# Kernel optimization log

Hardware: AMD Instinct MI355X
Metric: run time of the kernel (lower is better)

The kernel has to match this reference:

```python
import jax, jax.numpy as jnp
import numpy as np

MIN_CONTEXT_SIZE = 64
FUTURE_STEPS = 12


def setup_inputs() -> dict:
    key = jax.random.key(0)
    k1, k2, k3 = jax.random.split(key, 3)
    B, T, E, C = 32, 256, 256, 256
    embeddings = jax.random.normal(k1, (B, T, E), dtype=jnp.float32)
    contexts = jax.random.normal(k2, (B, T, C), dtype=jnp.float32)
    # Bilinear comparator weight, scaled like a typical linear init
    W = jax.random.normal(k3, (E, C), dtype=jnp.float32) * (1.0 / np.sqrt(E).astype(np.float32))
    return {"embeddings": embeddings, "contexts": contexts, "W": W}


def reference(embeddings, contexts, W):
    B, T, E = embeddings.shape
    log_probs = []
    for step in range(FUTURE_STEPS):
        emb = embeddings[:, MIN_CONTEXT_SIZE + step:T]          # (B, S, E)
        ctx = contexts[:, MIN_CONTEXT_SIZE - 1:T - step - 1]    # (B, S, C)
        S = T - step - MIN_CONTEXT_SIZE
        # all-pairs bilinear scores: score[b,s,j,t] = emb[b,s] @ W @ ctx[j,t]
        proj = jnp.einsum('bse,ec->bsc', emb, W)                # (B, S, C)
        scores = jnp.einsum('bsc,jtc->bsjt', proj, ctx)         # (B, S, B, S)
        flat = scores.reshape(B * S, B * S)
        positives = jnp.diagonal(flat).reshape(B, S)            # matched (b,s) pairs
        lse = jax.nn.logsumexp(scores.reshape(B, S, B * S), axis=-1)
        lse = lse - jnp.log(jnp.asarray(B * S, dtype=scores.dtype))
        log_probs.append((positives - lse).reshape(-1))
    flat_log_probs = jnp.concatenate(log_probs, axis=0)
    return -flat_log_probs.mean()
```

## Files before the change

kernel.cpp:

```cpp
#include <hip/hip_runtime.h>
#include <hip/hip_bf16.h>


#define NROW 6144
#define TAIL0 181
#define NTERMS 71616.0f

typedef __attribute__((ext_vector_type(8))) short short8;
typedef __attribute__((ext_vector_type(4))) float f32x4;

__device__ __forceinline__ ushort f2bf(float f) {
  union { float f; uint32_t u; } v; v.f = f;
  uint32_t u = v.u;
  return (ushort)((u + 0x7FFFu + ((u >> 16) & 1u)) >> 16);
}
__device__ __forceinline__ float b2f(ushort h) {
  union { uint32_t u; float f; } v; v.u = ((uint32_t)h) << 16; return v.f;
}

__device__ __forceinline__ void gload16(const ushort* g, ushort* l) {
  __builtin_amdgcn_global_load_lds((const __attribute__((address_space(1))) void*)g,
                                   (__attribute__((address_space(3))) void*)l, 16, 0, 0);
}

__global__ void k_castW(const float* __restrict__ W, ushort* __restrict__ Wt) {
  int c = blockIdx.x, e = threadIdx.x;
  Wt[c * 256 + e] = f2bf(W[e * 256 + c]);
}

__global__ void k_castX(const float* __restrict__ ctx, ushort* __restrict__ X) {
  int c = blockIdx.x;
  int j = c & 31, t = c >> 5;
  const float4* src = (const float4*)(ctx + ((size_t)(j * 256 + 63 + t)) * 256);
  float4 f = src[threadIdx.x];
  ushort4 o;
  o.x = f2bf(f.x); o.y = f2bf(f.y); o.z = f2bf(f.z); o.w = f2bf(f.w);
  ((ushort4*)(X + (size_t)c * 256))[threadIdx.x] = o;
}

__global__ __launch_bounds__(256) void k_proj(const float* __restrict__ emb,
                                              const ushort* __restrict__ Wt,
                                              ushort* __restrict__ P) {
  __shared__ ushort Al[16 * 256];
  int tid = threadIdx.x;
  int rt = blockIdx.x;
#pragma unroll
  for (int q = 0; q < 4; ++q) {
    int cc = tid + q * 256;
    int rw = cc >> 6, f4 = cc & 63;
    int u = rt * 16 + rw, b = u / 192, urow = u - b * 192;
    float4 f = *(const float4*)(emb + ((size_t)(b * 256 + 64 + urow)) * 256 + f4 * 4);
    ushort4 o;
    o.x = f2bf(f.x); o.y = f2bf(f.y); o.z = f2bf(f.z); o.w = f2bf(f.w);
    int c8 = f4 >> 1;
    *(ushort4*)&Al[rw * 256 + ((c8 ^ (rw & 7)) * 8) + (f4 & 1) * 4] = o;
  }
  __syncthreads();

  int w = tid >> 6, l = tid & 63;
  int fr = l & 15, kb = l >> 4;
  short8 af[8];
#pragma unroll
  for (int kk = 0; kk < 8; ++kk) {
    int c8 = kk * 4 + kb;
    af[kk] = *(const short8*)&Al[fr * 256 + (c8 ^ (fr & 7)) * 8];
  }
#pragma unroll
  for (int i = 0; i < 4; ++i) {
    int ct = w * 4 + i;
    const short8* bp = (const short8*)(Wt + (size_t)(ct * 16 + fr) * 256);
    f32x4 acc = {0.f, 0.f, 0.f, 0.f};
#pragma unroll
    for (int kk = 0; kk < 8; ++kk)
      acc = __builtin_amdgcn_mfma_f32_16x16x32_bf16(af[kk], bp[kk * 4 + kb], acc, 0, 0, 0);
#pragma unroll
    for (int r = 0; r < 4; ++r)
      P[(size_t)(rt * 16 + kb * 4 + r) * 256 + ct * 16 + fr] = f2bf(acc[r]);
  }
}

__global__ __launch_bounds__(256) void k_scores(const ushort* __restrict__ P,
                                                const ushort* __restrict__ X,
                                                float* __restrict__ sum0,
                                                float* __restrict__ tail,
                                                float* __restrict__ pos) {
  __shared__ ushort Al[128 * 32];
  __shared__ ushort Bl[128 * 32];
  int tid = threadIdx.x;
  int w = tid >> 6, l = tid & 63;
  int wr = w >> 1, wc = w & 1;
  int rowbase = blockIdx.x * 128;
  int colbase = blockIdx.y * 128;

  int c0 = w * 128 + l;
  int r0 = c0 >> 2, s0 = (c0 & 3) ^ ((c0 >> 3) & 3);
  int c1 = c0 + 64;
  int r1 = c1 >> 2, s1 = (c1 & 3) ^ ((c1 >> 3) & 3);
  const ushort* gA0 = P + (size_t)(rowbase + r0) * 256 + s0 * 8;
  const ushort* gA1 = P + (size_t)(rowbase + r1) * 256 + s1 * 8;
  const ushort* gB0 = X + (size_t)(colbase + r0) * 256 + s0 * 8;
  const ushort* gB1 = X + (size_t)(colbase + r1) * 256 + s1 * 8;
  ushort* lA0 = Al + (size_t)(w * 128) * 8;
  ushort* lA1 = Al + (size_t)(w * 128 + 64) * 8;
  ushort* lB0 = Bl + (size_t)(w * 128) * 8;
  ushort* lB1 = Bl + (size_t)(w * 128 + 64) * 8;

  int fr = l & 15, kb = l >> 4;
  int kbs = kb ^ ((fr >> 1) & 3);

  f32x4 acc[4][4];
#pragma unroll
  for (int m = 0; m < 4; ++m)
#pragma unroll
    for (int n = 0; n < 4; ++n) acc[m][n] = {0.f, 0.f, 0.f, 0.f};

  for (int kk = 0; kk < 8; ++kk) {
    gload16(gA0 + kk * 32, lA0);
    gload16(gA1 + kk * 32, lA1);
    gload16(gB0 + kk * 32, lB0);
    gload16(gB1 + kk * 32, lB1);
    __syncthreads();

    short8 af[4], bf[4];
#pragma unroll
    for (int m = 0; m < 4; ++m)
      af[m] = *(const short8*)&Al[(wr * 64 + m * 16 + fr) * 32 + kbs * 8];
#pragma unroll
    for (int n = 0; n < 4; ++n)
      bf[n] = *(const short8*)&Bl[(wc * 64 + n * 16 + fr) * 32 + kbs * 8];
#pragma unroll
    for (int m = 0; m < 4; ++m)
#pragma unroll
      for (int n = 0; n < 4; ++n)
        acc[m][n] = __builtin_amdgcn_mfma_f32_16x16x32_bf16(af[m], bf[n], acc[m][n], 0, 0, 0);
    if (kk < 7) __syncthreads();
  }

  int t0g = blockIdx.y * 4 + wc * 2;
#pragma unroll
  for (int m = 0; m < 4; ++m) {
    int rowg = rowbase + wr * 64 + m * 16 + kb * 4;
#pragma unroll
    for (int r = 0; r < 4; ++r) {
      int u = rowg + r;
      int b = u / 192;
      int urow = u - b * 192;
#pragma unroll
      for (int n = 0; n < 4; ++n) {
        int colg = colbase + wc * 64 + n * 16 + fr;
        int dt = urow - (colg >> 5);
        if ((colg & 31) == b && dt >= 0 && dt < 12)
          pos[u * 12 + dt] = acc[m][n][r];
      }
      float v0 = __expf(acc[m][0][r] - 64.f) + __expf(acc[m][1][r] - 64.f);
      float v1 = __expf(acc[m][2][r] - 64.f) + __expf(acc[m][3][r] - 64.f);
      v0 += __shfl_xor(v0, 1); v0 += __shfl_xor(v0, 2);
      v0 += __shfl_xor(v0, 4); v0 += __shfl_xor(v0, 8);
      v1 += __shfl_xor(v1, 1); v1 += __shfl_xor(v1, 2);
      v1 += __shfl_xor(v1, 4); v1 += __shfl_xor(v1, 8);
      if (fr == 0) {
        if (t0g + 1 < TAIL0) {
          atomicAdd(&sum0[u], v0 + v1);
        } else if (t0g < TAIL0) {
          atomicAdd(&sum0[u], v0);
          tail[(size_t)(t0g + 1 - TAIL0) * NROW + u] = v1;
        } else {
          tail[(size_t)(t0g - TAIL0) * NROW + u] = v0;
          tail[(size_t)(t0g + 1 - TAIL0) * NROW + u] = v1;
        }
      }
    }
  }
}

__global__ void k_loss(const float* __restrict__ sum0, const float* __restrict__ tail,
                       const float* __restrict__ pos, float* __restrict__ acc) {
  int u = blockIdx.x * 256 + threadIdx.x;
  int urow = u % 192;
  int smax = urow < 11 ? urow : 11;
  float denom = sum0[u];
  float local = 0.f;
  for (int s = 11; s >= 0; --s) {
    if (s < 11) denom += tail[(size_t)(10 - s) * NROW + u];
    if (s <= smax)
      local += pos[u * 12 + s] - 64.f - __logf(denom) + __logf(32.f * (float)(192 - s));
  }
  float v = local;
  v += __shfl_xor(v, 1);  v += __shfl_xor(v, 2);  v += __shfl_xor(v, 4);
  v += __shfl_xor(v, 8);  v += __shfl_xor(v, 16); v += __shfl_xor(v, 32);
  __shared__ float red[4];
  if ((threadIdx.x & 63) == 0) red[threadIdx.x >> 6] = v;
  __syncthreads();
  if (threadIdx.x == 0) atomicAdd(acc, red[0] + red[1] + red[2] + red[3]);
}

__global__ void k_final(const float* __restrict__ acc, float* __restrict__ out) {
  if (threadIdx.x == 0) out[0] = -acc[0] * (1.0f / NTERMS);
}

extern "C" void kernel_launch(void* const* d_in, const int* in_sizes, int n_in,
                              void* d_out, int out_size, void* d_ws, size_t ws_size,
                              hipStream_t stream) {
  const float* emb = (const float*)d_in[0];
  const float* ctx = (const float*)d_in[1];
  const float* W   = (const float*)d_in[2];
  char* ws = (char*)d_ws;
  ushort* P    = (ushort*)(ws + 0);
  ushort* X    = (ushort*)(ws + 3145728);
  ushort* Wt   = (ushort*)(ws + 6291456);
  float*  sum0 = (float*)(ws + 6422528);
  float*  acc  = (float*)(ws + 6447104);
  float*  tail = (float*)(ws + 6447360);
  float*  pos  = (float*)(ws + 6717696);

  hipMemsetAsync(sum0, 0, 24580, stream);

  k_castW<<<256, 256, 0, stream>>>(W, Wt);
  k_castX<<<6144, 64, 0, stream>>>(ctx, X);
  k_proj<<<384, 256, 0, stream>>>(emb, Wt, P);
  k_scores<<<dim3(48, 48), 256, 0, stream>>>(P, X, sum0, tail, pos);
  k_loss<<<24, 256, 0, stream>>>(sum0, tail, pos, acc);
  k_final<<<1, 64, 0, stream>>>(acc, (float*)d_out);
}
```

Before: 78.43 us.

## Double-buffer LDS tiles in score GEMM, merge cast kernels, streamline exp reduction

The score GEMM now uses two LDS buffers, so the next K-slice is fetched while MFMAs run on the current one, hiding global load latency. The W and context cast kernels are merged into one launch to save a kernel launch. The exp is rewritten as exp2 with a fused multiply-add shift. Column blocks lying entirely before the tail region take a single-reduction path that does one shuffle tree and one atomic per row instead of two. Double buffering doubles LDS use per block, which may lower occupancy.

```diff
diff --git a/kernel.cpp b/kernel.cpp
--- a/kernel.cpp
+++ b/kernel.cpp
@@ -1,10 +1,13 @@
 #include <hip/hip_runtime.h>
 #include <hip/hip_bf16.h>
+#include <math.h>
 
 
 #define NROW 6144
 #define TAIL0 181
 #define NTERMS 71616.0f
+#define LOG2E 1.44269504088896340736f
+#define SHIFT2 92.33248261689366f
 
 typedef __attribute__((ext_vector_type(8))) short short8;
 typedef __attribute__((ext_vector_type(4))) float f32x4;
@@ -17,25 +20,32 @@
 __device__ __forceinline__ float b2f(ushort h) {
   union { uint32_t u; float f; } v; v.u = ((uint32_t)h) << 16; return v.f;
 }
+__device__ __forceinline__ float expsh(float x) {
+  return exp2f(fmaf(x, LOG2E, -SHIFT2));
+}
 
 __device__ __forceinline__ void gload16(const ushort* g, ushort* l) {
   __builtin_amdgcn_global_load_lds((const __attribute__((address_space(1))) void*)g,
                                    (__attribute__((address_space(3))) void*)l, 16, 0, 0);
 }
 
-__global__ void k_castW(const float* __restrict__ W, ushort* __restrict__ Wt) {
-  int c = blockIdx.x, e = threadIdx.x;
-  Wt[c * 256 + e] = f2bf(W[e * 256 + c]);
-}
-
-__global__ void k_castX(const float* __restrict__ ctx, ushort* __restrict__ X) {
-  int c = blockIdx.x;
-  int j = c & 31, t = c >> 5;
-  const float4* src = (const float4*)(ctx + ((size_t)(j * 256 + 63 + t)) * 256);
-  float4 f = src[threadIdx.x];
-  ushort4 o;
-  o.x = f2bf(f.x); o.y = f2bf(f.y); o.z = f2bf(f.z); o.w = f2bf(f.w);
-  ((ushort4*)(X + (size_t)c * 256))[threadIdx.x] = o;
+__global__ __launch_bounds__(256) void k_cast(const float* __restrict__ ctx,
+                                              const float* __restrict__ W,
+                                              ushort* __restrict__ X,
+                                              ushort* __restrict__ Wt) {
+  int bi = blockIdx.x;
+  if (bi < 1536) {
+    int idx = bi * 256 + threadIdx.x;
+    int row = idx >> 6, f4 = idx & 63;
+    int j = row & 31, t = row >> 5;
+    float4 f = *(const float4*)(ctx + ((size_t)(j * 256 + 63 + t)) * 256 + f4 * 4);
+    ushort4 o;
+    o.x = f2bf(f.x); o.y = f2bf(f.y); o.z = f2bf(f.z); o.w = f2bf(f.w);
+    ((ushort4*)(X + (size_t)row * 256))[f4] = o;
+  } else {
+    int c = bi - 1536, e = threadIdx.x;
+    Wt[c * 256 + e] = f2bf(W[e * 256 + c]);
+  }
 }
 
 __global__ __launch_bounds__(256) void k_proj(const float* __restrict__ emb,
@@ -84,8 +94,8 @@
                                                 float* __restrict__ sum0,
                                                 float* __restrict__ tail,
                                                 float* __restrict__ pos) {
-  __shared__ ushort Al[128 * 32];
-  __shared__ ushort Bl[128 * 32];
+  __shared__ ushort Al[2][128 * 32];
+  __shared__ ushort Bl[2][128 * 32];
   int tid = threadIdx.x;
   int w = tid >> 6, l = tid & 63;
   int wr = w >> 1, wc = w & 1;
@@ -100,10 +110,8 @@
   const ushort* gA1 = P + (size_t)(rowbase + r1) * 256 + s1 * 8;
   const ushort* gB0 = X + (size_t)(colbase + r0) * 256 + s0 * 8;
   const ushort* gB1 = X + (size_t)(colbase + r1) * 256 + s1 * 8;
-  ushort* lA0 = Al + (size_t)(w * 128) * 8;
-  ushort* lA1 = Al + (size_t)(w * 128 + 64) * 8;
-  ushort* lB0 = Bl + (size_t)(w * 128) * 8;
-  ushort* lB1 = Bl + (size_t)(w * 128 + 64) * 8;
+  ushort* lA0 = &Al[0][w * 1024];
+  ushort* lB0 = &Bl[0][w * 1024];
 
   int fr = l & 15, kb = l >> 4;
   int kbs = kb ^ ((fr >> 1) & 3);
@@ -114,29 +122,40 @@
 #pragma unroll
     for (int n = 0; n < 4; ++n) acc[m][n] = {0.f, 0.f, 0.f, 0.f};
 
+  gload16(gA0, lA0);
+  gload16(gA1, lA0 + 512);
+  gload16(gB0, lB0);
+  gload16(gB1, lB0 + 512);
+  __syncthreads();
+
   for (int kk = 0; kk < 8; ++kk) {
-    gload16(gA0 + kk * 32, lA0);
-    gload16(gA1 + kk * 32, lA1);
-    gload16(gB0 + kk * 32, lB0);
-    gload16(gB1 + kk * 32, lB1);
-    __syncthreads();
-
+    int cur = kk & 1;
+    if (kk < 7) {
+      int nb = cur ^ 1;
+      gload16(gA0 + (kk + 1) * 32, lA0 + nb * 4096);
+      gload16(gA1 + (kk + 1) * 32, lA0 + nb * 4096 + 512);
+      gload16(gB0 + (kk + 1) * 32, lB0 + nb * 4096);
+      gload16(gB1 + (kk + 1) * 32, lB0 + nb * 4096 + 512);
+    }
+    const ushort* Ab = &Al[cur][0];
+    const ushort* Bb = &Bl[cur][0];
     short8 af[4], bf[4];
 #pragma unroll
     for (int m = 0; m < 4; ++m)
-      af[m] = *(const short8*)&Al[(wr * 64 + m * 16 + fr) * 32 + kbs * 8];
+      af[m] = *(const short8*)&Ab[(wr * 64 + m * 16 + fr) * 32 + kbs * 8];
 #pragma unroll
     for (int n = 0; n < 4; ++n)
-      bf[n] = *(const short8*)&Bl[(wc * 64 + n * 16 + fr) * 32 + kbs * 8];
+      bf[n] = *(const short8*)&Bb[(wc * 64 + n * 16 + fr) * 32 + kbs * 8];
 #pragma unroll
     for (int m = 0; m < 4; ++m)
 #pragma unroll
       for (int n = 0; n < 4; ++n)
         acc[m][n] = __builtin_amdgcn_mfma_f32_16x16x32_bf16(af[m], bf[n], acc[m][n], 0, 0, 0);
-    if (kk < 7) __syncthreads();
+    __syncthreads();
   }
 
   int t0g = blockIdx.y * 4 + wc * 2;
+  bool all0 = blockIdx.y < 45;
 #pragma unroll
   for (int m = 0; m < 4; ++m) {
     int rowg = rowbase + wr * 64 + m * 16 + kb * 4;
@@ -152,21 +171,29 @@
         if ((colg & 31) == b && dt >= 0 && dt < 12)
           pos[u * 12 + dt] = acc[m][n][r];
       }
-      float v0 = __expf(acc[m][0][r] - 64.f) + __expf(acc[m][1][r] - 64.f);
-      float v1 = __expf(acc[m][2][r] - 64.f) + __expf(acc[m][3][r] - 64.f);
-      v0 += __shfl_xor(v0, 1); v0 += __shfl_xor(v0, 2);
-      v0 += __shfl_xor(v0, 4); v0 += __shfl_xor(v0, 8);
-      v1 += __shfl_xor(v1, 1); v1 += __shfl_xor(v1, 2);
-      v1 += __shfl_xor(v1, 4); v1 += __shfl_xor(v1, 8);
-      if (fr == 0) {
-        if (t0g + 1 < TAIL0) {
-          atomicAdd(&sum0[u], v0 + v1);
-        } else if (t0g < TAIL0) {
-          atomicAdd(&sum0[u], v0);
-          tail[(size_t)(t0g + 1 - TAIL0) * NROW + u] = v1;
-        } else {
-          tail[(size_t)(t0g - TAIL0) * NROW + u] = v0;
-          tail[(size_t)(t0g + 1 - TAIL0) * NROW + u] = v1;
+      if (all0) {
+        float v = expsh(acc[m][0][r]) + expsh(acc[m][1][r]) +
+                  expsh(acc[m][2][r]) + expsh(acc[m][3][r]);
+        v += __shfl_xor(v, 1); v += __shfl_xor(v, 2);
+        v += __shfl_xor(v, 4); v += __shfl_xor(v, 8);
+        if (fr == 0) atomicAdd(&sum0[u], v);
+      } else {
+        float v0 = expsh(acc[m][0][r]) + expsh(acc[m][1][r]);
+        float v1 = expsh(acc[m][2][r]) + expsh(acc[m][3][r]);
+        v0 += __shfl_xor(v0, 1); v0 += __shfl_xor(v0, 2);
+        v0 += __shfl_xor(v0, 4); v0 += __shfl_xor(v0, 8);
+        v1 += __shfl_xor(v1, 1); v1 += __shfl_xor(v1, 2);
+        v1 += __shfl_xor(v1, 4); v1 += __shfl_xor(v1, 8);
+        if (fr == 0) {
+          if (t0g + 1 < TAIL0) {
+            atomicAdd(&sum0[u], v0 + v1);
+          } else if (t0g < TAIL0) {
+            atomicAdd(&sum0[u], v0);
+            tail[(size_t)(t0g + 1 - TAIL0) * NROW + u] = v1;
+          } else {
+            tail[(size_t)(t0g - TAIL0) * NROW + u] = v0;
+            tail[(size_t)(t0g + 1 - TAIL0) * NROW + u] = v1;
+          }
         }
       }
     }
@@ -215,8 +242,7 @@
 
   hipMemsetAsync(sum0, 0, 24580, stream);
 
-  k_castW<<<256, 256, 0, stream>>>(W, Wt);
-  k_castX<<<6144, 64, 0, stream>>>(ctx, X);
+  k_cast<<<1792, 256, 0, stream>>>(ctx, W, X, Wt);
   k_proj<<<384, 256, 0, stream>>>(emb, Wt, P);
   k_scores<<<dim3(48, 48), 256, 0, stream>>>(P, X, sum0, tail, pos);
   k_loss<<<24, 256, 0, stream>>>(sum0, tail, pos, acc);
```

Result: slower. 84.13 us (+7.3%).
